# Kernel optimization log

Hardware: AMD Instinct MI355X
Metric: run time of the kernel (lower is better)

Reference implementation:

```python
import jax, jax.numpy as jnp
import numpy as np

B, S, D, H = 2, 2048, 1024, 16
HD = D // H  # 64


def setup_inputs() -> dict:
    key = jax.random.key(0)
    ks = jax.random.split(key, 11)
    w_scale = 1.0 / np.sqrt(D)
    Q = jax.random.normal(ks[0], (B, S, D), jnp.float32)
    K = jax.random.normal(ks[1], (B, S, D), jnp.float32)
    V = jax.random.normal(ks[2], (B, S, D), jnp.float32)
    # causal mask: True = masked (matches torch masked_fill semantics)
    mask = ~jnp.tril(jnp.ones((S, S), bool))[None, None]  # [1,1,S,S]
    # RoPE freqs (precomputed cos/sin of freqs_cis, shape [S, HD//2])
    inv_freq = 1.0 / (10000.0 ** (jnp.arange(0, HD, 2, dtype=jnp.float32) / HD))
    angles = jnp.arange(S, dtype=jnp.float32)[:, None] * inv_freq[None, :]
    freqs_cos, freqs_sin = jnp.cos(angles), jnp.sin(angles)
    wq = jax.random.normal(ks[3], (D, D), jnp.float32) * w_scale
    wk = jax.random.normal(ks[4], (D, D), jnp.float32) * w_scale
    wv = jax.random.normal(ks[5], (D, D), jnp.float32) * w_scale
    wo = jax.random.normal(ks[6], (D, D), jnp.float32) * w_scale
    bq = jax.random.normal(ks[7], (D,), jnp.float32) * 0.01
    bk = jax.random.normal(ks[8], (D,), jnp.float32) * 0.01
    bv = jax.random.normal(ks[9], (D,), jnp.float32) * 0.01
    bo = jax.random.normal(ks[10], (D,), jnp.float32) * 0.01
    return {"Q": Q, "K": K, "V": V, "mask": mask,
            "freqs_cos": freqs_cos, "freqs_sin": freqs_sin,
            "wq": wq, "bq": bq, "wk": wk, "bk": bk,
            "wv": wv, "bv": bv, "wo": wo, "bo": bo}


def _rope(x, cos, sin):
    # x: [B,S,H,HD]; complex pairing of adjacent dims as in view_as_complex
    xr, xi = x[..., 0::2], x[..., 1::2]
    c = cos[None, :, None, :]
    s = sin[None, :, None, :]
    out_r = xr * c - xi * s
    out_i = xr * s + xi * c
    return jnp.stack([out_r, out_i], axis=-1).reshape(x.shape)


def reference(Q, K, V, mask, freqs_cos, freqs_sin, wq, bq, wk, bk, wv, bv, wo, bo):
    b, s, d = Q.shape
    h = H
    hd = d // h
    q = (Q @ wq.T + bq).reshape(b, s, h, hd)
    k = (K @ wk.T + bk).reshape(b, s, h, hd)
    v = (V @ wv.T + bv).reshape(b, s, h, hd)
    q = _rope(q, freqs_cos, freqs_sin)
    k = _rope(k, freqs_cos, freqs_sin)
    q = q.transpose(0, 2, 1, 3)  # [B,H,S,HD]
    k = k.transpose(0, 2, 1, 3)
    v = v.transpose(0, 2, 1, 3)
    scale = jnp.sqrt(jnp.float32(hd))
    energy = jnp.einsum('bhqd,bhkd->bhqk', q, k) / scale
    energy = jnp.where(mask, jnp.float32(-1e10), energy)
    attn = jax.nn.softmax(energy, axis=-1)  # dropout p=0.0 -> identity
    out = jnp.einsum('bhqk,bhkd->bhqd', attn, v)
    out = out.transpose(0, 2, 1, 3).reshape(b, s, d)
    return out @ wo.T + bo
```

## Files before the change

kernel.cpp:

```cpp
#include <hip/hip_runtime.h>
#include <stdint.h>

#define NB 2
#define NS 2048
#define ND 1024
#define NH 16
#define NHD 64
#define NM (NB*NS)

typedef __bf16 bf16;
typedef float f32x4 __attribute__((ext_vector_type(4)));
typedef __bf16 bf16x8 __attribute__((ext_vector_type(8)));
typedef __bf16 bf16x4 __attribute__((ext_vector_type(4)));

#define MFMA16(a,b,c) __builtin_amdgcn_mfma_f32_16x16x32_bf16(a,b,c,0,0,0)

__device__ __forceinline__ void gld_lds16(const bf16* g, bf16* l) {
  __builtin_amdgcn_global_load_lds((const __attribute__((address_space(1))) void*)g,
                                   (__attribute__((address_space(3))) void*)l,
                                   16, 0, 0);
}

__device__ __forceinline__ void block_sync_lds() {
  asm volatile("s_waitcnt lgkmcnt(0)\n\ts_barrier" ::: "memory");
}

__global__ __launch_bounds__(256)
void cvt7(const float* __restrict__ s0, const float* __restrict__ s1,
          const float* __restrict__ s2, const float* __restrict__ s3,
          const float* __restrict__ s4, const float* __restrict__ s5,
          const float* __restrict__ s6, bf16* __restrict__ dst) {
  const int t = blockIdx.y;
  const float* s = (t == 0) ? s0 : (t == 1) ? s1 : (t == 2) ? s2 :
                   (t == 3) ? s3 : (t == 4) ? s4 : (t == 5) ? s5 : s6;
  const int n4 = (t < 3) ? (1 << 20) : (1 << 18);
  const size_t eoff = (t < 3) ? ((size_t)t << 22) : ((size_t)12 << 20) + ((size_t)(t - 3) << 20);
  int i = blockIdx.x * blockDim.x + threadIdx.x;
  if (i >= n4) return;
  float4 v = ((const float4*)s)[i];
  bf16x4 o = { (bf16)v.x, (bf16)v.y, (bf16)v.z, (bf16)v.w };
  ((bf16x4*)(dst + eoff))[i] = o;
}

template<int MODE>
__global__ __launch_bounds__(256)
void gemm_nt(const bf16* __restrict__ A, const bf16* __restrict__ W,
             const float* __restrict__ b0, const float* __restrict__ b1,
             const float* __restrict__ b2,
             const float* __restrict__ fc, const float* __restrict__ fs,
             bf16* __restrict__ obf, bf16* __restrict__ vtp,
             float* __restrict__ of) {
  constexpr int K = ND;
  constexpr int BN = 64;
  constexpr int NJ = 2;
  constexpr int ITB = 2;
  __shared__ __align__(16) bf16 As[128 * 64];
  __shared__ __align__(16) bf16 Bs[BN * 64];
  const int tid = threadIdx.x;
  const int w = tid >> 6, lane = tid & 63;

  const int id = blockIdx.x;
  const int xcd = id & 7, r = id >> 3;
  int t, nt, mt;
  if (MODE == 0) { t = r >> 6; const int rem = r & 63; nt = rem & 15; mt = xcd + 8 * (rem >> 4); }
  else           { t = 0;                              nt = r & 15;   mt = xcd + 8 * (r >> 4);   }

  const bf16* Ab = A + (size_t)t * ((size_t)NM * K);
  const bf16* Wb = W + (size_t)t * ((size_t)ND * K);
  const float* bias = (t == 0) ? b0 : (t == 1) ? b1 : b2;
  const int wr = (w >> 1) * 64, wc = (w & 1) * 32;
  f32x4 acc[4][NJ] = {};

  const int swsrc = (((lane & 7) ^ ((lane >> 3) & 7)) << 3);
  const bf16* ga = Ab + (size_t)(mt * 128 + w * 8 + (lane >> 3)) * K + swsrc;
  const bf16* gb = Wb + (size_t)(nt * BN + w * 8 + (lane >> 3)) * K + swsrc;

  for (int k0 = 0; k0 < K; k0 += 64) {
    __syncthreads();
#pragma unroll
    for (int it = 0; it < 4; ++it)
      gld_lds16(ga + (size_t)(it * 32) * K + k0, As + (it * 4 + w) * 512);
#pragma unroll
    for (int it = 0; it < ITB; ++it)
      gld_lds16(gb + (size_t)(it * 32) * K + k0, Bs + (it * 4 + w) * 512);
    __syncthreads();

#pragma unroll
    for (int ks = 0; ks < 2; ++ks) {
      bf16x8 af[4], bfr[NJ];
#pragma unroll
      for (int i = 0; i < 4; ++i) {
        const int row = wr + i * 16 + (lane & 15);
        af[i] = *(const bf16x8*)&As[row * 64 +
                 (((ks * 4 + (lane >> 4)) ^ (lane & 7)) << 3)];
      }
#pragma unroll
      for (int j = 0; j < NJ; ++j) {
        const int row = wc + j * 16 + (lane & 15);
        bfr[j] = *(const bf16x8*)&Bs[row * 64 +
                  (((ks * 4 + (lane >> 4)) ^ (lane & 7)) << 3)];
      }
#pragma unroll
      for (int i = 0; i < 4; ++i)
#pragma unroll
        for (int j = 0; j < NJ; ++j)
          acc[i][j] = MFMA16(af[i], bfr[j], acc[i][j]);
    }
  }

#pragma unroll
  for (int i = 0; i < 4; ++i) {
#pragma unroll
    for (int j = 0; j < NJ; ++j) {
      const int gcol = nt * BN + wc + j * 16 + (lane & 15);
      const float bv = bias[gcol];
      if (MODE == 0 && t == 2) {
        const int s0g = mt * 128 + wr + i * 16 + (lane >> 4) * 4;
        const int b = s0g >> 11, s = s0g & (NS - 1);
        const int h = gcol >> 6, hd = gcol & 63;
        bf16x4 pk = { (bf16)(acc[i][j][0] + bv), (bf16)(acc[i][j][1] + bv),
                      (bf16)(acc[i][j][2] + bv), (bf16)(acc[i][j][3] + bv) };
        *(bf16x4*)&vtp[((size_t)(b * NH + h) * NHD + hd) * NS + s] = pk;
        continue;
      }
#pragma unroll
      for (int r4 = 0; r4 < 4; ++r4) {
        const int grow = mt * 128 + wr + i * 16 + (lane >> 4) * 4 + r4;
        float v = acc[i][j][r4] + bv;
        if (MODE == 0) {
          const int b = grow >> 11, s = grow & (NS - 1);
          const int h = gcol >> 6, hd = gcol & 63;
          float pv = __shfl_xor(v, 1);
          const int ii = hd >> 1;
          float c  = fc[(s << 5) + ii];
          float sn = fs[(s << 5) + ii];
          v = ((hd & 1) == 0) ? (v * c - pv * sn) : (pv * sn + v * c);
          if (t == 0) v *= 0.18033688011112042f;
          obf[(size_t)t * ((size_t)NM * ND) +
              (((size_t)(b * NH + h) * NS + s) * NHD + hd)] = (bf16)v;
        } else {
          of[(size_t)grow * ND + gcol] = v;
        }
      }
    }
  }
}

__device__ __forceinline__ void attn_tile(
    const bf16* __restrict__ Ksh, const bf16* __restrict__ Vsh,
    bf16* __restrict__ Pw, const bf16x8* qf, f32x4* o,
    float& m, float& l, int qi, int kk0, bool diag, int qrow, int grp) {
  const int s7 = qrow & 7;
  f32x4 sc[4] = {};
  __builtin_amdgcn_s_setprio(1);
#pragma unroll
  for (int ch = 0; ch < 2; ++ch)
#pragma unroll
    for (int cb = 0; cb < 4; ++cb) {
      bf16x8 kf = *(const bf16x8*)
        &Ksh[(cb * 16 + qrow) * 64 + (((ch * 4 + grp) ^ s7) << 3)];
      sc[cb] = MFMA16(kf, qf[ch], sc[cb]);
    }
  __builtin_amdgcn_s_setprio(0);

  if (diag) {
#pragma unroll
    for (int cb = 0; cb < 4; ++cb)
#pragma unroll
      for (int r = 0; r < 4; ++r)
        if (kk0 + cb * 16 + grp * 4 + r > qi) sc[cb][r] = -1e30f;
  }

  float a0 = fmaxf(fmaxf(sc[0][0], sc[0][1]), fmaxf(sc[0][2], sc[0][3]));
  float a1 = fmaxf(fmaxf(sc[1][0], sc[1][1]), fmaxf(sc[1][2], sc[1][3]));
  float a2 = fmaxf(fmaxf(sc[2][0], sc[2][1]), fmaxf(sc[2][2], sc[2][3]));
  float a3 = fmaxf(fmaxf(sc[3][0], sc[3][1]), fmaxf(sc[3][2], sc[3][3]));
  float pm = fmaxf(fmaxf(a0, a1), fmaxf(a2, a3));

  if (__any(pm > m + 8.f)) {
    float px = fmaxf(pm, __shfl_xor(pm, 16));
    px = fmaxf(px, __shfl_xor(px, 32));
    const float mn = fmaxf(m, px);
    const float scl = exp2f(m - mn);
    m = mn;
    l *= scl;
#pragma unroll
    for (int hb = 0; hb < 4; ++hb)
#pragma unroll
      for (int r = 0; r < 4; ++r) o[hb][r] *= scl;
  }

#pragma unroll
  for (int cb = 0; cb < 4; ++cb) {
    bf16x4 pk;
#pragma unroll
    for (int r = 0; r < 4; ++r) {
      float p = exp2f(sc[cb][r] - m);
      l += p;
      pk[r] = (bf16)p;
    }
    *(bf16x4*)&Pw[qrow * 64 + (((((cb << 1) | (grp >> 1)) ^ s7) << 3)) +
                  ((grp & 1) << 2)] = pk;
  }

  __builtin_amdgcn_s_setprio(1);
#pragma unroll
  for (int ch = 0; ch < 2; ++ch) {
    bf16x8 pa = *(const bf16x8*)
      &Pw[qrow * 64 + (((ch * 4 + grp) ^ s7) << 3)];
#pragma unroll
    for (int hb = 0; hb < 4; ++hb) {
      bf16x8 vf = *(const bf16x8*)
        &Vsh[(hb * 16 + qrow) * 64 + (((ch * 4 + grp) ^ s7) << 3)];
      o[hb] = MFMA16(vf, pa, o[hb]);
    }
  }
  __builtin_amdgcn_s_setprio(0);
}

__global__ __launch_bounds__(512, 4)
void attn_k(const bf16* __restrict__ q, const bf16* __restrict__ k,
            const bf16* __restrict__ vt, bf16* __restrict__ out) {
  __shared__ __align__(16) char smem[81920];
  bf16* KV = (bf16*)smem;
  bf16* Pr = (bf16*)(smem + 65536);
  auto MO = (float(*)[2][16][68])smem;
  auto ML = (float(*)[2][16][2])(smem + 36864);

  const int tid = threadIdx.x;
  const int w = tid >> 6, lane = tid & 63;
  const int h = w >> 2, wl = w & 3;
  const int qrow = lane & 15, grp = lane >> 4;
  const int bh = blockIdx.x, j = blockIdx.y;
  const int b = bh >> 4, hh = bh & (NH - 1);
  const int tA = j, tB = 31 - j;

  const bf16* qb = q + (size_t)bh * NS * NHD;
  const bf16* kb = k + (size_t)bh * NS * NHD;
  const bf16* vb = vt + (size_t)bh * NHD * NS;

  const int nA = (j >= h) ? (((j - h) >> 1) + 1) : 0;
  const int nB = (((31 - j) - h) >> 1) + 1;
  const int len = nA + nB;

  const int q0A = tA * 64 + wl * 16, q0B = tB * 64 + wl * 16;
  bf16x8 qfA[2], qfB[2];
#pragma unroll
  for (int ch = 0; ch < 2; ++ch) {
    qfA[ch] = *(const bf16x8*)&qb[(size_t)(q0A + qrow) * NHD + ch * 32 + grp * 8];
    qfB[ch] = *(const bf16x8*)&qb[(size_t)(q0B + qrow) * NHD + ch * 32 + grp * 8];
  }

  f32x4 oA[4] = {}, oB[4] = {};
  float mA = -1e30f, lA = 0.f, mB = -1e30f, lB = 0.f;

  const int local = tid & 255;
  const int r0 = local >> 3;
  const int c0 = (local & 7) * 8;
  const int sw = (((local & 7) ^ (r0 & 7)) << 3);

  bf16* Pw = Pr + w * 1024;
  auto Kb = [&](int buf) { return KV + ((h * 2 + buf) * 2 + 0) * 4096; };
  auto Vb = [&](int buf) { return KV + ((h * 2 + buf) * 2 + 1) * 4096; };

  bf16x8 ka0, ka1, va0, va1;
  auto load_round = [&](int r) {
    const bool isA = r < nA;
    const int kt = isA ? (h + 2 * r) : (h + 2 * (r - nA));
    const int kk0 = kt * 64;
    ka0 = *(const bf16x8*)&kb[(size_t)(kk0 + r0) * NHD + c0];
    ka1 = *(const bf16x8*)&kb[(size_t)(kk0 + r0 + 32) * NHD + c0];
    va0 = *(const bf16x8*)&vb[(size_t)r0 * NS + kk0 + c0];
    va1 = *(const bf16x8*)&vb[(size_t)(r0 + 32) * NS + kk0 + c0];
  };
  auto store_tile = [&](int buf) {
    bf16* Ksc = Kb(buf);
    bf16* Vsc = Vb(buf);
    *(bf16x8*)&Ksc[r0 * 64 + sw]        = ka0;
    *(bf16x8*)&Ksc[(r0 + 32) * 64 + sw] = ka1;
    *(bf16x8*)&Vsc[r0 * 64 + sw]        = va0;
    *(bf16x8*)&Vsc[(r0 + 32) * 64 + sw] = va1;
  };

  load_round(0);
  store_tile(0);
  load_round(1);
  block_sync_lds();

  for (int r = 0; r < 17; ++r) {
    const int cur = r & 1;
    const bool act = r < len;
    if (r + 1 < len) store_tile(cur ^ 1);
    if (r + 2 < len) load_round(r + 2);
    if (act) {
      const bool isA = r < nA;
      const int kt = isA ? (h + 2 * r) : (h + 2 * (r - nA));
      if (isA)
        attn_tile(Kb(cur), Vb(cur), Pw, qfA, oA, mA, lA,
                  q0A + qrow, kt * 64, kt == tA, qrow, grp);
      else
        attn_tile(Kb(cur), Vb(cur), Pw, qfB, oB, mB, lB,
                  q0B + qrow, kt * 64, kt == tB, qrow, grp);
    }
    block_sync_lds();
  }

  lA += __shfl_xor(lA, 16); lA += __shfl_xor(lA, 32);
  lB += __shfl_xor(lB, 16); lB += __shfl_xor(lB, 32);

  __syncthreads();

  if (h == 1) {
#pragma unroll
    for (int hb = 0; hb < 4; ++hb) {
      *(f32x4*)&MO[wl][0][qrow][hb * 16 + grp * 4] = oA[hb];
      *(f32x4*)&MO[wl][1][qrow][hb * 16 + grp * 4] = oB[hb];
    }
    if (grp == 0) {
      ML[wl][0][qrow][0] = mA; ML[wl][0][qrow][1] = lA;
      ML[wl][1][qrow][0] = mB; ML[wl][1][qrow][1] = lB;
    }
  }
  __syncthreads();

  if (h == 0) {
#pragma unroll
    for (int sub = 0; sub < 2; ++sub) {
      const float m0 = sub ? mB : mA, l0 = sub ? lB : lA;
      const f32x4* o0 = sub ? oB : oA;
      const float m1 = ML[wl][sub][qrow][0], l1 = ML[wl][sub][qrow][1];
      const float mm = fmaxf(m0, m1);
      const float s0 = exp2f(m0 - mm), s1 = exp2f(m1 - mm);
      const float inv = 1.f / (l0 * s0 + l1 * s1);
      const int s = (sub ? q0B : q0A) + qrow;
      bf16* op = out + (size_t)(b * NS + s) * ND + hh * NHD + grp * 4;
#pragma unroll
      for (int hb = 0; hb < 4; ++hb) {
        f32x4 o1 = *(const f32x4*)&MO[wl][sub][qrow][hb * 16 + grp * 4];
        bf16x4 ov = { (bf16)((o0[hb][0] * s0 + o1[0] * s1) * inv),
                      (bf16)((o0[hb][1] * s0 + o1[1] * s1) * inv),
                      (bf16)((o0[hb][2] * s0 + o1[2] * s1) * inv),
                      (bf16)((o0[hb][3] * s0 + o1[3] * s1) * inv) };
        *(bf16x4*)&op[hb * 16] = ov;
      }
    }
  }
}

extern "C" void kernel_launch(void* const* d_in, const int* in_sizes, int n_in,
                              void* d_out, int out_size, void* d_ws, size_t ws_size,
                              hipStream_t stream) {
  const float* Q  = (const float*)d_in[0];
  const float* K  = (const float*)d_in[1];
  const float* V  = (const float*)d_in[2];
  const float* fc = (const float*)d_in[4];
  const float* fs = (const float*)d_in[5];
  const float* wq = (const float*)d_in[6];
  const float* bq = (const float*)d_in[7];
  const float* wk = (const float*)d_in[8];
  const float* bk = (const float*)d_in[9];
  const float* wv = (const float*)d_in[10];
  const float* bv = (const float*)d_in[11];
  const float* wo = (const float*)d_in[12];
  const float* bo = (const float*)d_in[13];
  float* out = (float*)d_out;
  bf16* ws = (bf16*)d_ws;

  const size_t MB_ = 1024 * 1024;
  bf16* Qbf  = ws;
  bf16* Wqkv = ws + 12 * MB_;
  bf16* Wo   = ws + 15 * MB_;
  bf16* qp   = ws + 16 * MB_;
  bf16* kp   = ws + 20 * MB_;
  bf16* vtp  = ws + 28 * MB_;
  bf16* aout = ws + 32 * MB_;

  cvt7<<<dim3(4096, 7), 256, 0, stream>>>(Q, K, V, wq, wk, wv, wo, ws);

  gemm_nt<0><<<1536, 256, 0, stream>>>(Qbf, Wqkv, bq, bk, bv, fc, fs,
                                       qp, vtp, nullptr);

  attn_k<<<dim3(32, 16), 512, 0, stream>>>(qp, kp, vtp, aout);

  gemm_nt<1><<<512, 256, 0, stream>>>(aout, Wo, bo, bo, bo, fc, fs,
                                      nullptr, nullptr, out);
}
```

Before: 117.3 us.

## Load V fragments directly from global in attention; shrink output GEMM M-tile

Attention no longer stages V tiles through shared memory; each wave loads its V MFMA operands straight from global memory at the start of each tile, and LDS usage drops from 80KB to 48KB. This removes the V LDS store/load traffic and may raise occupancy, at the cost of redundant uncoalesced global reads across waves. The output projection GEMM uses a 64-row M tile and doubles the grid to improve CU fill.

```diff
diff --git a/kernel.cpp b/kernel.cpp
--- a/kernel.cpp
+++ b/kernel.cpp
@@ -51,10 +51,13 @@
              bf16* __restrict__ obf, bf16* __restrict__ vtp,
              float* __restrict__ of) {
   constexpr int K = ND;
+  constexpr int BM = (MODE == 0) ? 128 : 64;
   constexpr int BN = 64;
+  constexpr int MI = (MODE == 0) ? 4 : 2;
   constexpr int NJ = 2;
+  constexpr int ITA = (MODE == 0) ? 4 : 2;
   constexpr int ITB = 2;
-  __shared__ __align__(16) bf16 As[128 * 64];
+  __shared__ __align__(16) bf16 As[BM * 64];
   __shared__ __align__(16) bf16 Bs[BN * 64];
   const int tid = threadIdx.x;
   const int w = tid >> 6, lane = tid & 63;
@@ -68,17 +71,17 @@
   const bf16* Ab = A + (size_t)t * ((size_t)NM * K);
   const bf16* Wb = W + (size_t)t * ((size_t)ND * K);
   const float* bias = (t == 0) ? b0 : (t == 1) ? b1 : b2;
-  const int wr = (w >> 1) * 64, wc = (w & 1) * 32;
-  f32x4 acc[4][NJ] = {};
+  const int wr = (w >> 1) * (BM / 2), wc = (w & 1) * 32;
+  f32x4 acc[MI][NJ] = {};
 
   const int swsrc = (((lane & 7) ^ ((lane >> 3) & 7)) << 3);
-  const bf16* ga = Ab + (size_t)(mt * 128 + w * 8 + (lane >> 3)) * K + swsrc;
+  const bf16* ga = Ab + (size_t)(mt * BM + w * 8 + (lane >> 3)) * K + swsrc;
   const bf16* gb = Wb + (size_t)(nt * BN + w * 8 + (lane >> 3)) * K + swsrc;
 
   for (int k0 = 0; k0 < K; k0 += 64) {
     __syncthreads();
 #pragma unroll
-    for (int it = 0; it < 4; ++it)
+    for (int it = 0; it < ITA; ++it)
       gld_lds16(ga + (size_t)(it * 32) * K + k0, As + (it * 4 + w) * 512);
 #pragma unroll
     for (int it = 0; it < ITB; ++it)
@@ -87,9 +90,9 @@
 
 #pragma unroll
     for (int ks = 0; ks < 2; ++ks) {
-      bf16x8 af[4], bfr[NJ];
-#pragma unroll
-      for (int i = 0; i < 4; ++i) {
+      bf16x8 af[MI], bfr[NJ];
+#pragma unroll
+      for (int i = 0; i < MI; ++i) {
         const int row = wr + i * 16 + (lane & 15);
         af[i] = *(const bf16x8*)&As[row * 64 +
                  (((ks * 4 + (lane >> 4)) ^ (lane & 7)) << 3)];
@@ -101,7 +104,7 @@
                   (((ks * 4 + (lane >> 4)) ^ (lane & 7)) << 3)];
       }
 #pragma unroll
-      for (int i = 0; i < 4; ++i)
+      for (int i = 0; i < MI; ++i)
 #pragma unroll
         for (int j = 0; j < NJ; ++j)
           acc[i][j] = MFMA16(af[i], bfr[j], acc[i][j]);
@@ -109,13 +112,13 @@
   }
 
 #pragma unroll
-  for (int i = 0; i < 4; ++i) {
+  for (int i = 0; i < MI; ++i) {
 #pragma unroll
     for (int j = 0; j < NJ; ++j) {
       const int gcol = nt * BN + wc + j * 16 + (lane & 15);
       const float bv = bias[gcol];
       if (MODE == 0 && t == 2) {
-        const int s0g = mt * 128 + wr + i * 16 + (lane >> 4) * 4;
+        const int s0g = mt * BM + wr + i * 16 + (lane >> 4) * 4;
         const int b = s0g >> 11, s = s0g & (NS - 1);
         const int h = gcol >> 6, hd = gcol & 63;
         bf16x4 pk = { (bf16)(acc[i][j][0] + bv), (bf16)(acc[i][j][1] + bv),
@@ -125,7 +128,7 @@
       }
 #pragma unroll
       for (int r4 = 0; r4 < 4; ++r4) {
-        const int grow = mt * 128 + wr + i * 16 + (lane >> 4) * 4 + r4;
+        const int grow = mt * BM + wr + i * 16 + (lane >> 4) * 4 + r4;
         float v = acc[i][j][r4] + bv;
         if (MODE == 0) {
           const int b = grow >> 11, s = grow & (NS - 1);
@@ -147,10 +150,19 @@
 }
 
 __device__ __forceinline__ void attn_tile(
-    const bf16* __restrict__ Ksh, const bf16* __restrict__ Vsh,
+    const bf16* __restrict__ Ksh, const bf16* __restrict__ vg,
     bf16* __restrict__ Pw, const bf16x8* qf, f32x4* o,
     float& m, float& l, int qi, int kk0, bool diag, int qrow, int grp) {
   const int s7 = qrow & 7;
+
+  bf16x8 vf[2][4];
+#pragma unroll
+  for (int ch = 0; ch < 2; ++ch)
+#pragma unroll
+    for (int hb = 0; hb < 4; ++hb)
+      vf[ch][hb] = *(const bf16x8*)
+        &vg[(size_t)(hb * 16 + qrow) * NS + ch * 32 + grp * 8];
+
   f32x4 sc[4] = {};
   __builtin_amdgcn_s_setprio(1);
 #pragma unroll
@@ -209,11 +221,8 @@
     bf16x8 pa = *(const bf16x8*)
       &Pw[qrow * 64 + (((ch * 4 + grp) ^ s7) << 3)];
 #pragma unroll
-    for (int hb = 0; hb < 4; ++hb) {
-      bf16x8 vf = *(const bf16x8*)
-        &Vsh[(hb * 16 + qrow) * 64 + (((ch * 4 + grp) ^ s7) << 3)];
-      o[hb] = MFMA16(vf, pa, o[hb]);
-    }
+    for (int hb = 0; hb < 4; ++hb)
+      o[hb] = MFMA16(vf[ch][hb], pa, o[hb]);
   }
   __builtin_amdgcn_s_setprio(0);
 }
@@ -221,9 +230,9 @@
 __global__ __launch_bounds__(512, 4)
 void attn_k(const bf16* __restrict__ q, const bf16* __restrict__ k,
             const bf16* __restrict__ vt, bf16* __restrict__ out) {
-  __shared__ __align__(16) char smem[81920];
-  bf16* KV = (bf16*)smem;
-  bf16* Pr = (bf16*)(smem + 65536);
+  __shared__ __align__(16) char smem[49152];
+  bf16* Kv = (bf16*)smem;
+  bf16* Pr = (bf16*)(smem + 32768);
   auto MO = (float(*)[2][16][68])smem;
   auto ML = (float(*)[2][16][2])(smem + 36864);
 
@@ -260,26 +269,20 @@
   const int sw = (((local & 7) ^ (r0 & 7)) << 3);
 
   bf16* Pw = Pr + w * 1024;
-  auto Kb = [&](int buf) { return KV + ((h * 2 + buf) * 2 + 0) * 4096; };
-  auto Vb = [&](int buf) { return KV + ((h * 2 + buf) * 2 + 1) * 4096; };
-
-  bf16x8 ka0, ka1, va0, va1;
+  auto Kb = [&](int buf) { return Kv + (h * 2 + buf) * 4096; };
+  auto ktile = [&](int r) { const bool isA = r < nA;
+                            return isA ? (h + 2 * r) : (h + 2 * (r - nA)); };
+
+  bf16x8 ka0, ka1;
   auto load_round = [&](int r) {
-    const bool isA = r < nA;
-    const int kt = isA ? (h + 2 * r) : (h + 2 * (r - nA));
-    const int kk0 = kt * 64;
+    const int kk0 = ktile(r) * 64;
     ka0 = *(const bf16x8*)&kb[(size_t)(kk0 + r0) * NHD + c0];
     ka1 = *(const bf16x8*)&kb[(size_t)(kk0 + r0 + 32) * NHD + c0];
-    va0 = *(const bf16x8*)&vb[(size_t)r0 * NS + kk0 + c0];
-    va1 = *(const bf16x8*)&vb[(size_t)(r0 + 32) * NS + kk0 + c0];
   };
   auto store_tile = [&](int buf) {
     bf16* Ksc = Kb(buf);
-    bf16* Vsc = Vb(buf);
     *(bf16x8*)&Ksc[r0 * 64 + sw]        = ka0;
     *(bf16x8*)&Ksc[(r0 + 32) * 64 + sw] = ka1;
-    *(bf16x8*)&Vsc[r0 * 64 + sw]        = va0;
-    *(bf16x8*)&Vsc[(r0 + 32) * 64 + sw] = va1;
   };
 
   load_round(0);
@@ -294,12 +297,13 @@
     if (r + 2 < len) load_round(r + 2);
     if (act) {
       const bool isA = r < nA;
-      const int kt = isA ? (h + 2 * r) : (h + 2 * (r - nA));
+      const int kt = ktile(r);
+      const bf16* vg = vb + kt * 64;
       if (isA)
-        attn_tile(Kb(cur), Vb(cur), Pw, qfA, oA, mA, lA,
+        attn_tile(Kb(cur), vg, Pw, qfA, oA, mA, lA,
                   q0A + qrow, kt * 64, kt == tA, qrow, grp);
       else
-        attn_tile(Kb(cur), Vb(cur), Pw, qfB, oB, mB, lB,
+        attn_tile(Kb(cur), vg, Pw, qfB, oB, mB, lB,
                   q0B + qrow, kt * 64, kt == tB, qrow, grp);
     }
     block_sync_lds();
@@ -382,6 +386,6 @@
 
   attn_k<<<dim3(32, 16), 512, 0, stream>>>(qp, kp, vtp, aout);
 
-  gemm_nt<1><<<512, 256, 0, stream>>>(aout, Wo, bo, bo, bo, fc, fs,
-                                      nullptr, nullptr, out);
-}
+  gemm_nt<1><<<1024, 256, 0, stream>>>(aout, Wo, bo, bo, bo, fc, fs,
+                                       nullptr, nullptr, out);
+}
```

Measured after the change: 186.4 us. +58.8%, slower.
